# Kernel optimization log

Measured on AMD Instinct MI355X. Metric: run time of the kernel, lower is better.

## Reference

```python
import jax, jax.numpy as jnp
import numpy as np

B, N, DIM = 4, 1024, 768
H, HD = 12, DIM // 12
GP = 49
MLP = 3072


def _layernorm(x, w, b, eps=1e-5):
    mu = x.mean(axis=-1, keepdims=True)
    var = ((x - mu) ** 2).mean(axis=-1, keepdims=True)
    return (x - mu) * jax.lax.rsqrt(var + eps) * w + b


def setup_inputs() -> dict:
    key = jax.random.key(0)
    ks = jax.random.split(key, 12)
    s = 0.02
    return {
        "x": jax.random.normal(ks[0], (B, N, DIM), jnp.float32),
        "ln1_w": jnp.ones((DIM,), jnp.float32),
        "ln1_b": jnp.zeros((DIM,), jnp.float32),
        "qkv_w": jax.random.normal(ks[1], (DIM, 3 * DIM), jnp.float32) * s,
        "qkv_b": jnp.zeros((3 * DIM,), jnp.float32),
        "proj_w": jax.random.normal(ks[2], (DIM, DIM), jnp.float32) * s,
        "proj_b": jnp.zeros((DIM,), jnp.float32),
        "gp_w": jax.random.normal(ks[3], (GP, DIM), jnp.float32) * s,  # nn.Linear(dim, gp_num).weight, shape (gp_num, dim)
        "alpha": jax.random.normal(ks[4], (1, H, 1, 1), jnp.float32),
        "ln2_w": jnp.ones((DIM,), jnp.float32),
        "ln2_b": jnp.zeros((DIM,), jnp.float32),
        "ff1_w": jax.random.normal(ks[5], (DIM, MLP), jnp.float32) * s,
        "ff1_b": jnp.zeros((MLP,), jnp.float32),
        "ff2_w": jax.random.normal(ks[6], (MLP, DIM), jnp.float32) * s,
        "ff2_b": jnp.zeros((DIM,), jnp.float32),
    }


def reference(x, ln1_w, ln1_b, qkv_w, qkv_b, proj_w, proj_b, gp_w, alpha,
              ln2_w, ln2_b, ff1_w, ff1_b, ff2_w, ff2_b):
    b, n, _ = x.shape
    # --- attention branch ---
    xn = _layernorm(x, ln1_w, ln1_b)
    qkv = xn @ qkv_w + qkv_b                                 # [b,n,3*dim]
    q, k, v = jnp.split(qkv, 3, axis=-1)
    to_heads = lambda t: t.reshape(b, n, H, HD).transpose(0, 2, 1, 3)  # [b,h,n,hd]
    q, k, v = to_heads(q), to_heads(k), to_heads(v)
    scale = HD ** -0.5
    attn = jnp.einsum('bhnd,bhmd->bhnm', q, k) * scale       # raw scores
    # group weights: view (gp_num, dim) -> (h, gp_num, hd) (row-major, same as torch .view)
    gp = gp_w.reshape(H, GP, HD)
    gw = jnp.einsum('bhnd,hmd->bhnm', v, gp)                 # [b,h,n,gp]
    gw = jax.nn.gelu(gw, approximate=False)
    gw = jax.nn.softmax(gw, axis=-1)
    gw = jnp.einsum('bhnm,bhkm->bhnk', gw, gw)               # [b,h,n,n]
    attn = jax.nn.softmax(attn * gw, axis=-1)
    a = jax.nn.sigmoid(alpha)
    attn = (1.0 - a) * attn + a * gw
    attn = attn / (attn.sum(axis=2, keepdims=True) + 1e-8)   # note: dim=2 (column renorm), faithful to source
    out = jnp.einsum('bhnm,bhmd->bhnd', attn, v)
    out = out.transpose(0, 2, 1, 3).reshape(b, n, DIM)
    out = out @ proj_w + proj_b
    x = out + x
    # --- FFN branch ---
    xn = _layernorm(x, ln2_w, ln2_b)
    hdn = jax.nn.gelu(xn @ ff1_w + ff1_b, approximate=False)
    x = (hdn @ ff2_w + ff2_b) + x
    return x
```

## Files before the change

### kernel.cpp

```cpp
#include <hip/hip_runtime.h>
#include <hip/hip_bf16.h>
#include <math.h>

#define DEVI __device__ __forceinline__

typedef __bf16 bf16x8 __attribute__((ext_vector_type(8)));
typedef float f32x4 __attribute__((ext_vector_type(4)));
typedef unsigned int u32x4 __attribute__((ext_vector_type(4)));
typedef float f32x4v __attribute__((ext_vector_type(4)));
typedef unsigned short u16;

DEVI u16 f2bf(float f) {
    __hip_bfloat16 h = __float2bfloat16(f);
    return __builtin_bit_cast(u16, h);
}
DEVI float bf2f(u16 u) {
    unsigned int x = ((unsigned int)u) << 16;
    return __builtin_bit_cast(float, x);
}
DEVI float gelu_f(float x) {
    float y = 0.7978845608f * (x + 0.044715f * x * x * x);
    float e = __expf(2.f * y);
    float t = 1.f - 2.f / (e + 1.f);
    return 0.5f * x * (1.f + t);
}
DEVI float sigm(float x) { return 1.f / (1.f + __expf(-x)); }

DEVI bf16x8 ldfrag(const u16* p) {
    return __builtin_bit_cast(bf16x8, *reinterpret_cast<const u32x4*>(p));
}

DEVI void gload_lds16(const u16* g, u16* l) {
    __builtin_amdgcn_global_load_lds(
        (const __attribute__((address_space(1))) void*)g,
        (__attribute__((address_space(3))) void*)l, 16, 0, 0);
}

DEVI void stage8(const u16* gbase, long long stride, u16* lds, int lane) {
    int r = lane >> 3;
    int kg = (lane & 7) ^ r;
    gload_lds16(gbase + (long long)r * stride + kg * 8, lds);
}
DEVI bf16x8 fragsw(const u16* tile, int rr, int k) {
    return ldfrag(&tile[rr * 64 + ((k ^ (rr & 7)) << 3)]);
}

__global__ __launch_bounds__(256) void tcast_k(const float* __restrict__ in, u16* __restrict__ out,
                                               int R, int C) {
    __shared__ float tile[32][33];
    int c0 = blockIdx.x * 32, r0 = blockIdx.y * 32;
    for (int ry = threadIdx.y; ry < 32; ry += 8)
        tile[ry][threadIdx.x] = in[(long long)(r0 + ry) * C + c0 + threadIdx.x];
    __syncthreads();
    for (int cy = threadIdx.y; cy < 32; cy += 8)
        out[(long long)(c0 + cy) * R + r0 + threadIdx.x] = f2bf(tile[threadIdx.x][cy]);
}

__global__ __launch_bounds__(256) void ln_k(const float* __restrict__ parts, int nparts, long long pstride,
                                            const float* __restrict__ bias2, const float* __restrict__ in2,
                                            const float* __restrict__ w, const float* __restrict__ b,
                                            u16* __restrict__ outbf, float* __restrict__ x1out,
                                            float* __restrict__ zfill) {
    int row = blockIdx.x;
    if (zfill && row < 192) zfill[row * 256 + threadIdx.x] = 0.f;
    long long ro = (long long)row * 768;
    __shared__ float lds1[4], lds2[4];
    float v[3];
    float s = 0.f, sq = 0.f;
#pragma unroll
    for (int j = 0; j < 3; j++) {
        int c = threadIdx.x + j * 256;
        float x = 0.f;
        for (int p = 0; p < nparts; p++) x += parts[p * pstride + ro + c];
        if (bias2) x += bias2[c];
        if (in2) x += in2[ro + c];
        v[j] = x; s += x; sq += x * x;
    }
    if (x1out) {
#pragma unroll
        for (int j = 0; j < 3; j++) x1out[ro + threadIdx.x + j * 256] = v[j];
    }
    for (int off = 32; off; off >>= 1) { s += __shfl_down(s, off); sq += __shfl_down(sq, off); }
    int wid = threadIdx.x >> 6;
    if ((threadIdx.x & 63) == 0) { lds1[wid] = s; lds2[wid] = sq; }
    __syncthreads();
    s = lds1[0] + lds1[1] + lds1[2] + lds1[3];
    sq = lds2[0] + lds2[1] + lds2[2] + lds2[3];
    float mu = s * (1.f / 768.f);
    float var = sq * (1.f / 768.f) - mu * mu;
    float rs = rsqrtf(var + 1e-5f);
#pragma unroll
    for (int j = 0; j < 3; j++) {
        int c = threadIdx.x + j * 256;
        outbf[ro + c] = f2bf((v[j] - mu) * rs * w[c] + b[c]);
    }
}

struct GemmP {
    const u16* A; const u16* B;
    float* outF; u16* outB;
    const float* bias;
    u16* qh; u16* kh; u16* vh;
    int K, lda, ldb, ldc;
    long long pstride;
    int epi;
    int splits;
};

__global__ __launch_bounds__(128) void gemm_bt2(GemmP p) {
    __shared__ u16 As[64 * 64];
    __shared__ u16 Bs[128 * 64];
    const int tid = threadIdx.x, lane = tid & 63, wave = tid >> 6;
    const int l16 = lane & 15, qd = lane >> 4;
    const int bn0 = blockIdx.x * 128, bm0 = blockIdx.y * 64;
    const int wn0 = wave * 64;
    const int kc = p.K / p.splits;
    const int kbeg = blockIdx.z * kc, kend = kbeg + kc;
    f32x4 acc[4][4] = {};
    for (int k0 = kbeg; k0 < kend; k0 += 64) {
        __syncthreads();
#pragma unroll
        for (int t = 0; t < 4; t++) {
            int rowg = wave * 32 + t * 8;
            stage8(p.A + (long long)(bm0 + rowg) * p.lda + k0, p.lda, As + rowg * 64, lane);
        }
#pragma unroll
        for (int t = 0; t < 8; t++) {
            int rowg = wave * 64 + t * 8;
            stage8(p.B + (long long)(bn0 + rowg) * p.ldb + k0, p.ldb, Bs + rowg * 64, lane);
        }
        __syncthreads();
#pragma unroll
        for (int s = 0; s < 2; s++) {
            bf16x8 af[4], bv[4];
#pragma unroll
            for (int i = 0; i < 4; i++) af[i] = fragsw(As, i * 16 + l16, s * 4 + qd);
#pragma unroll
            for (int j = 0; j < 4; j++) bv[j] = fragsw(Bs, wn0 + j * 16 + l16, s * 4 + qd);
#pragma unroll
            for (int i = 0; i < 4; i++)
#pragma unroll
                for (int j = 0; j < 4; j++)
                    acc[i][j] = __builtin_amdgcn_mfma_f32_16x16x32_bf16(af[i], bv[j], acc[i][j], 0, 0, 0);
        }
    }
#pragma unroll
    for (int i = 0; i < 4; i++)
#pragma unroll
        for (int j = 0; j < 4; j++)
#pragma unroll
            for (int r = 0; r < 4; r++) {
                int row = bm0 + i * 16 + qd * 4 + r;
                int col = bn0 + wn0 + j * 16 + l16;
                float v = acc[i][j][r];
                if (p.epi == 0) {
                    p.outF[(long long)blockIdx.z * p.pstride + (long long)row * p.ldc + col] = v;
                } else if (p.epi == 2) {
                    p.outB[(long long)row * p.ldc + col] = f2bf(gelu_f(v + p.bias[col]));
                } else {
                    v += p.bias[col];
                    int sect = col / 768, cc = col % 768;
                    int h = cc >> 6, d = cc & 63;
                    int b = row >> 10, n = row & 1023;
                    long long o = ((long long)(b * 12 + h) * 1024 + n) * 64 + d;
                    if (sect == 0) p.qh[o] = f2bf(v * 0.125f);
                    else if (sect == 1) p.kh[o] = f2bf(v);
                    else p.vh[o] = f2bf(v);
                }
            }
}

__global__ __launch_bounds__(256) void gpcast_k(const float* __restrict__ gp_w, u16* __restrict__ gpB) {
    int h = blockIdx.x;
    for (int i = threadIdx.x; i < 4096; i += 256) {
        int m = i >> 6, d = i & 63;
        float v = (m < 49) ? gp_w[h * 3136 + m * 64 + d] : 0.f;
        gpB[h * 4096 + i] = f2bf(v);
    }
}

__global__ __launch_bounds__(256) void gw0m_k(const u16* __restrict__ vh, const u16* __restrict__ gpB,
                                              u16* __restrict__ gwn, float* __restrict__ Wt) {
    {
        long long zi = ((long long)blockIdx.y * 16 + blockIdx.x) * 256 + threadIdx.x;
        Wt[zi] = 0.f;
    }
    __shared__ u16 As[64 * 64];
    __shared__ u16 Bs[64 * 64];
    const int tid = threadIdx.x, lane = tid & 63, wave = tid >> 6;
    const int l16 = lane & 15, qd = lane >> 4;
    const int z = blockIdx.y, n0 = blockIdx.x * 64, h = z % 12;
    const u16* vz = vh + ((long long)z * 1024 + n0) * 64;
    const u16* gz = gpB + h * 4096;
#pragma unroll
    for (int t = 0; t < 2; t++) {
        int rowg = wave * 16 + t * 8;
        stage8(vz + (long long)rowg * 64, 64, As + rowg * 64, lane);
        stage8(gz + (long long)rowg * 64, 64, Bs + rowg * 64, lane);
    }
    __syncthreads();
    f32x4 acc[4] = {};
#pragma unroll
    for (int s = 0; s < 2; s++) {
        bf16x8 af = fragsw(As, wave * 16 + l16, s * 4 + qd);
#pragma unroll
        for (int j = 0; j < 4; j++) {
            bf16x8 bv = fragsw(Bs, j * 16 + l16, s * 4 + qd);
            acc[j] = __builtin_amdgcn_mfma_f32_16x16x32_bf16(af, bv, acc[j], 0, 0, 0);
        }
    }
    float ex[4][4];
#pragma unroll
    for (int r = 0; r < 4; r++) {
        float mx = -1e30f;
        float gv[4];
#pragma unroll
        for (int j = 0; j < 4; j++) {
            int col = j * 16 + l16;
            float g = gelu_f(acc[j][r]);
            gv[j] = g;
            if (col < 49) mx = fmaxf(mx, g);
            else gv[j] = -1e30f;
        }
        mx = fmaxf(mx, __shfl_xor(mx, 1)); mx = fmaxf(mx, __shfl_xor(mx, 2));
        mx = fmaxf(mx, __shfl_xor(mx, 4)); mx = fmaxf(mx, __shfl_xor(mx, 8));
        float s = 0.f;
#pragma unroll
        for (int j = 0; j < 4; j++) {
            int col = j * 16 + l16;
            float e = (col < 49) ? __expf(gv[j] - mx) : 0.f;
            ex[r][j] = e;
            s += e;
        }
        s += __shfl_xor(s, 1); s += __shfl_xor(s, 2);
        s += __shfl_xor(s, 4); s += __shfl_xor(s, 8);
        float inv = 1.f / s;
        int row = wave * 16 + qd * 4 + r;
        long long o = ((long long)z * 1024 + n0 + row) * 64;
#pragma unroll
        for (int j = 0; j < 4; j++)
            gwn[o + j * 16 + l16] = f2bf(ex[r][j] * inv);
    }
}

__global__ __launch_bounds__(256) void attn_tg4(const u16* __restrict__ qh, const u16* __restrict__ kh,
                                                const u16* __restrict__ gwn, u16* __restrict__ e,
                                                float* __restrict__ rowsumE) {
    __shared__ u16 As[128 * 64];
    __shared__ u16 Bs[128 * 64];
    const int tid = threadIdx.x, lane = tid & 63, wave = tid >> 6;
    const int l16 = lane & 15, qd = lane >> 4;
    const int bn0 = blockIdx.x * 128, bm0 = blockIdx.y * 128, z = blockIdx.z;
    const int wm0 = (wave >> 1) * 64, wn0 = (wave & 1) * 64;
    const u16* qz = qh + (long long)z * 65536;
    const u16* kz = kh + (long long)z * 65536;
    const u16* gz = gwn + (long long)z * 65536;
    f32x4 accS[4][4] = {};
    f32x4 accG[4][4] = {};
#pragma unroll
    for (int t = 0; t < 4; t++) {
        int rowg = wave * 32 + t * 8;
        stage8(qz + (long long)(bm0 + rowg) * 64, 64, As + rowg * 64, lane);
        stage8(kz + (long long)(bn0 + rowg) * 64, 64, Bs + rowg * 64, lane);
    }
    __syncthreads();
#pragma unroll
    for (int s = 0; s < 2; s++) {
        bf16x8 af[4], bv[4];
#pragma unroll
        for (int i = 0; i < 4; i++) af[i] = fragsw(As, wm0 + i * 16 + l16, s * 4 + qd);
#pragma unroll
        for (int j = 0; j < 4; j++) bv[j] = fragsw(Bs, wn0 + j * 16 + l16, s * 4 + qd);
#pragma unroll
        for (int i = 0; i < 4; i++)
#pragma unroll
            for (int j = 0; j < 4; j++)
                accS[i][j] = __builtin_amdgcn_mfma_f32_16x16x32_bf16(af[i], bv[j], accS[i][j], 0, 0, 0);
    }
    __syncthreads();
#pragma unroll
    for (int t = 0; t < 4; t++) {
        int rowg = wave * 32 + t * 8;
        stage8(gz + (long long)(bm0 + rowg) * 64, 64, As + rowg * 64, lane);
        stage8(gz + (long long)(bn0 + rowg) * 64, 64, Bs + rowg * 64, lane);
    }
    __syncthreads();
#pragma unroll
    for (int s = 0; s < 2; s++) {
        bf16x8 af[4], bv[4];
#pragma unroll
        for (int i = 0; i < 4; i++) af[i] = fragsw(As, wm0 + i * 16 + l16, s * 4 + qd);
#pragma unroll
        for (int j = 0; j < 4; j++) bv[j] = fragsw(Bs, wn0 + j * 16 + l16, s * 4 + qd);
#pragma unroll
        for (int i = 0; i < 4; i++)
#pragma unroll
            for (int j = 0; j < 4; j++)
                accG[i][j] = __builtin_amdgcn_mfma_f32_16x16x32_bf16(af[i], bv[j], accG[i][j], 0, 0, 0);
    }
    long long zoff = (long long)z * 1048576;
#pragma unroll
    for (int i = 0; i < 4; i++)
#pragma unroll
        for (int r = 0; r < 4; r++) {
            int row = bm0 + wm0 + i * 16 + qd * 4 + r;
            float rs = 0.f;
#pragma unroll
            for (int j = 0; j < 4; j++) {
                int col = bn0 + wn0 + j * 16 + l16;
                float ev = __expf(accS[i][j][r] * accG[i][j][r]);
                e[zoff + (long long)row * 1024 + col] = f2bf(ev);
                rs += ev;
            }
            rs += __shfl_xor(rs, 1); rs += __shfl_xor(rs, 2);
            rs += __shfl_xor(rs, 4); rs += __shfl_xor(rs, 8);
            if (l16 == 0) atomicAdd(&rowsumE[z * 1024 + row], rs);
        }
}

__global__ __launch_bounds__(256) void combine2_k(const u16* __restrict__ gwn, const float* __restrict__ alpha,
                                                  float* __restrict__ colsum) {
    int z = blockIdx.x, h = z % 12;
    int j = threadIdx.x & 63, part = threadIdx.x >> 6;
    __shared__ float lds[4][64];
    __shared__ float Sl[64];
    float s = 0.f;
    for (int i = 0; i < 256; i++)
        s += bf2f(gwn[((long long)z * 1024 + part * 256 + i) * 64 + j]);
    lds[part][j] = s;
    __syncthreads();
    if (threadIdx.x < 64)
        Sl[threadIdx.x] = lds[0][threadIdx.x] + lds[1][threadIdx.x] + lds[2][threadIdx.x] + lds[3][threadIdx.x];
    __syncthreads();
    float a = sigm(alpha[h]);
    for (int m = threadIdx.x; m < 1024; m += 256) {
        const u16* g = gwn + ((long long)z * 1024 + m) * 64;
        float dot = 0.f;
#pragma unroll 8
        for (int jj = 0; jj < 64; jj++) dot += bf2f(g[jj]) * Sl[jj];
        colsum[z * 1024 + m] = a * dot;
    }
}

__global__ __launch_bounds__(256) void colsumE_k(const u16* __restrict__ e, const float* __restrict__ rowsumE,
                                                 const float* __restrict__ alpha, float* __restrict__ colsum) {
    int z = blockIdx.x, h = z % 12;
    int n0 = blockIdx.y * 128;
    int grp = threadIdx.x & 127;
    int half = threadIdx.x >> 7;
    const u16* p = e + (long long)z * 1048576;
    const float* rs = rowsumE + z * 1024;
    float acc[8] = {};
    for (int n = n0 + half * 64; n < n0 + half * 64 + 64; n++) {
        unsigned int rw[4];
        *reinterpret_cast<u32x4*>(rw) = *reinterpret_cast<const u32x4*>(&p[(long long)n * 1024 + grp * 8]);
        float inv = 1.f / rs[n];
#pragma unroll
        for (int q = 0; q < 4; q++) {
            float lo = __builtin_bit_cast(float, rw[q] << 16);
            float hi = __builtin_bit_cast(float, rw[q] & 0xffff0000u);
            acc[2 * q] += lo * inv;
            acc[2 * q + 1] += hi * inv;
        }
    }
    __shared__ float part[2][128][8];
#pragma unroll
    for (int j = 0; j < 8; j++) part[half][grp][j] = acc[j];
    __syncthreads();
    if (half == 0) {
        float a = sigm(alpha[h]);
#pragma unroll
        for (int j = 0; j < 8; j++)
            atomicAdd(&colsum[z * 1024 + grp * 8 + j], (1.f - a) * (part[0][grp][j] + part[1][grp][j]));
    }
}

__global__ __launch_bounds__(256) void vpt_k(const u16* __restrict__ vh, const float* __restrict__ colsum,
                                             u16* __restrict__ vpt) {
    int z = blockIdx.y, m0 = blockIdx.x * 64;
    __shared__ float ts[64 * 65];
    int mi = threadIdx.x >> 6, d = threadIdx.x & 63;
    for (int rr = 0; rr < 16; rr++) {
        int row = rr * 4 + mi;
        ts[row * 65 + d] = bf2f(vh[((long long)z * 1024 + m0 + row) * 64 + d]);
    }
    __syncthreads();
    int mj = threadIdx.x & 63, d0 = threadIdx.x >> 6;
    for (int rr = 0; rr < 16; rr++) {
        int dd = rr * 4 + d0;
        float cs = colsum[z * 1024 + m0 + mj] + 1e-8f;
        vpt[((long long)z * 64 + dd) * 1024 + m0 + mj] = f2bf(ts[mj * 65 + dd] / cs);
    }
}

__global__ __launch_bounds__(256) void wgemm_k(const u16* __restrict__ gwn, const u16* __restrict__ vpt,
                                               float* __restrict__ Wt) {
    int z = blockIdx.y, n0 = blockIdx.x * 128;
    __shared__ u16 gs[128 * 64];
    __shared__ u16 vs2[64 * 128];
    for (int i = threadIdx.x; i < 128 * 64; i += 256) {
        int nn = i >> 6, j = i & 63;
        gs[i] = gwn[((long long)z * 1024 + n0 + nn) * 64 + j];
        int d = i >> 7, n2 = i & 127;
        vs2[i] = vpt[((long long)z * 64 + d) * 1024 + n0 + n2];
    }
    __syncthreads();
    int j = threadIdx.x & 63, dg = threadIdx.x >> 6;
    float acc[16] = {};
    for (int nn = 0; nn < 128; nn++) {
        float g = bf2f(gs[nn * 64 + j]);
#pragma unroll
        for (int i = 0; i < 16; i++) acc[i] += g * bf2f(vs2[(dg * 16 + i) * 128 + nn]);
    }
#pragma unroll
    for (int i = 0; i < 16; i++)
        atomicAdd(&Wt[((long long)z * 64 + dg * 16 + i) * 64 + j], acc[i]);
}

__global__ __launch_bounds__(256) void attn_out4(const u16* __restrict__ e, const u16* __restrict__ vpt,
                                                 const u16* __restrict__ gwn, const float* __restrict__ Wt,
                                                 const float* __restrict__ rowsumE,
                                                 const float* __restrict__ alpha, u16* __restrict__ out) {
    __shared__ u16 As[64 * 64];
    __shared__ u16 Bs[64 * 64];
    const int tid = threadIdx.x, lane = tid & 63, wave = tid >> 6;
    const int l16 = lane & 15, qd = lane >> 4;
    const int bm0 = blockIdx.x * 64, z = blockIdx.y;
    const int h = z % 12, b = z / 12;
    const u16* Pz = e + (long long)z * 1048576;
    const u16* vz = vpt + (long long)z * 65536;
    const int wr = wave * 16;
    f32x4 accP[4] = {};
    f32x4 accG[4] = {};
    for (int k0 = 0; k0 < 1024; k0 += 64) {
        __syncthreads();
#pragma unroll
        for (int t = 0; t < 2; t++) {
            int rowg = wave * 16 + t * 8;
            stage8(Pz + (long long)(bm0 + rowg) * 1024 + k0, 1024, As + rowg * 64, lane);
            stage8(vz + (long long)rowg * 1024 + k0, 1024, Bs + rowg * 64, lane);
        }
        __syncthreads();
#pragma unroll
        for (int s = 0; s < 2; s++) {
            bf16x8 af = fragsw(As, wr + l16, s * 4 + qd);
#pragma unroll
            for (int j = 0; j < 4; j++) {
                bf16x8 bv = fragsw(Bs, j * 16 + l16, s * 4 + qd);
                accP[j] = __builtin_amdgcn_mfma_f32_16x16x32_bf16(af, bv, accP[j], 0, 0, 0);
            }
        }
    }
    const u16* gz = gwn + (long long)z * 65536;
    const float* wz = Wt + (long long)z * 4096;
    __syncthreads();
#pragma unroll
    for (int t = 0; t < 2; t++) {
        int rowg = wave * 16 + t * 8;
        stage8(gz + (long long)(bm0 + rowg) * 64, 64, As + rowg * 64, lane);
    }
    {
        int row = tid >> 2, c0 = (tid & 3) * 16;
        const float* wrow = wz + row * 64;
#pragma unroll
        for (int j0 = 0; j0 < 16; j0++) {
            int j = c0 + j0;
            int pos = (((j >> 3) ^ (row & 7)) << 3) | (j & 7);
            Bs[row * 64 + pos] = f2bf(wrow[j]);
        }
    }
    __syncthreads();
#pragma unroll
    for (int s = 0; s < 2; s++) {
        bf16x8 af = fragsw(As, wr + l16, s * 4 + qd);
#pragma unroll
        for (int j = 0; j < 4; j++) {
            bf16x8 bv = fragsw(Bs, j * 16 + l16, s * 4 + qd);
            accG[j] = __builtin_amdgcn_mfma_f32_16x16x32_bf16(af, bv, accG[j], 0, 0, 0);
        }
    }
    float a = sigm(alpha[h]);
#pragma unroll
    for (int r = 0; r < 4; r++) {
        int n = bm0 + wr + qd * 4 + r;
        float sc = (1.f - a) / rowsumE[z * 1024 + n];
#pragma unroll
        for (int j = 0; j < 4; j++) {
            int d = j * 16 + l16;
            float v = sc * accP[j][r] + a * accG[j][r];
            out[((long long)(b * 1024 + n)) * 768 + h * 64 + d] = f2bf(v);
        }
    }
}

__global__ __launch_bounds__(256) void fuse2_k(const float* __restrict__ parts, long long pstride4,
                                               const float* __restrict__ bias, const float* __restrict__ x1,
                                               float* __restrict__ outp) {
    long long i4 = (long long)blockIdx.x * 256 + threadIdx.x;
    int c4 = (int)(i4 % 192);
    const f32x4v* p0 = (const f32x4v*)parts;
    f32x4v v = p0[i4] + p0[pstride4 + i4];
    f32x4v bb = ((const f32x4v*)bias)[c4];
    f32x4v xx = ((const f32x4v*)x1)[i4];
    ((f32x4v*)outp)[i4] = v + bb + xx;
}

extern "C" void kernel_launch(void* const* d_in, const int* in_sizes, int n_in,
                              void* d_out, int out_size, void* d_ws, size_t ws_size,
                              hipStream_t stream) {
    const float* x      = (const float*)d_in[0];
    const float* ln1_w  = (const float*)d_in[1];
    const float* ln1_b  = (const float*)d_in[2];
    const float* qkv_w  = (const float*)d_in[3];
    const float* qkv_b  = (const float*)d_in[4];
    const float* proj_w = (const float*)d_in[5];
    const float* proj_b = (const float*)d_in[6];
    const float* gp_w   = (const float*)d_in[7];
    const float* alpha  = (const float*)d_in[8];
    const float* ln2_w  = (const float*)d_in[9];
    const float* ln2_b  = (const float*)d_in[10];
    const float* ff1_w  = (const float*)d_in[11];
    const float* ff1_b  = (const float*)d_in[12];
    const float* ff2_w  = (const float*)d_in[13];
    const float* ff2_b  = (const float*)d_in[14];

    char* w = (char*)d_ws;
    size_t off = 0;
    auto alloc = [&](size_t bytes) { size_t r = off; off += (bytes + 255) & ~(size_t)255; return r; };

    u16*   xn_bf   = (u16*)(w + alloc(4096LL * 768 * 2));
    u16*   wqkv_t  = (u16*)(w + alloc(2304LL * 768 * 2));
    u16*   wproj_t = (u16*)(w + alloc(768LL * 768 * 2));
    u16*   wff1_t  = (u16*)(w + alloc(3072LL * 768 * 2));
    u16*   wff2_t  = (u16*)(w + alloc(768LL * 3072 * 2));
    u16*   gpB     = (u16*)(w + alloc(12LL * 64 * 64 * 2));
    u16*   qh      = (u16*)(w + alloc(48LL * 1024 * 64 * 2));
    u16*   kh      = (u16*)(w + alloc(48LL * 1024 * 64 * 2));
    u16*   vh      = (u16*)(w + alloc(48LL * 1024 * 64 * 2));
    u16*   gwn     = (u16*)(w + alloc(48LL * 1024 * 64 * 2));
    u16*   ebuf    = (u16*)(w + alloc(48LL * 1024 * 1024 * 2));
    float* rowsumE = (float*)(w + alloc(48LL * 1024 * 4));
    float* Wt      = (float*)(w + alloc(48LL * 64 * 64 * 4));
    float* colsum  = (float*)(w + alloc(48LL * 1024 * 4));
    u16*   vpt     = (u16*)(w + alloc(48LL * 64 * 1024 * 2));
    float* x1      = (float*)(w + alloc(4096LL * 768 * 4));
    u16*   attn_o  = (u16*)(w + alloc(4096LL * 768 * 2));
    u16*   xn2     = (u16*)(w + alloc(4096LL * 768 * 2));
    float* projP = (float*)ebuf;
    u16*   hmid  = (u16*)((char*)ebuf + 2 * 4096LL * 768 * 4);
    float* ff2P  = (float*)((char*)ebuf + 2 * 4096LL * 768 * 4 + 4096LL * 3072 * 2);

    dim3 blk(256);
    dim3 blk2(128);
    const long long PS = 4096LL * 768;

    tcast_k<<<dim3(72, 24), dim3(32, 8), 0, stream>>>(qkv_w, wqkv_t, 768, 2304);
    tcast_k<<<dim3(24, 24), dim3(32, 8), 0, stream>>>(proj_w, wproj_t, 768, 768);
    tcast_k<<<dim3(96, 24), dim3(32, 8), 0, stream>>>(ff1_w, wff1_t, 768, 3072);
    tcast_k<<<dim3(24, 96), dim3(32, 8), 0, stream>>>(ff2_w, wff2_t, 3072, 768);
    gpcast_k<<<dim3(12), blk, 0, stream>>>(gp_w, gpB);

    ln_k<<<dim3(4096), blk, 0, stream>>>(x, 1, 0, nullptr, nullptr, ln1_w, ln1_b, xn_bf, nullptr, rowsumE);

    {
        GemmP p = {xn_bf, wqkv_t, nullptr, nullptr, qkv_b, qh, kh, vh, 768, 768, 768, 0, 0, 4, 1};
        gemm_bt2<<<dim3(18, 64, 1), blk2, 0, stream>>>(p);
    }

    gw0m_k<<<dim3(16, 48), blk, 0, stream>>>(vh, gpB, gwn, Wt);

    attn_tg4<<<dim3(8, 8, 48), blk, 0, stream>>>(qh, kh, gwn, ebuf, rowsumE);

    combine2_k<<<dim3(48), blk, 0, stream>>>(gwn, alpha, colsum);
    colsumE_k<<<dim3(48, 8), blk, 0, stream>>>(ebuf, rowsumE, alpha, colsum);

    vpt_k<<<dim3(16, 48), blk, 0, stream>>>(vh, colsum, vpt);

    wgemm_k<<<dim3(8, 48), blk, 0, stream>>>(gwn, vpt, Wt);

    attn_out4<<<dim3(16, 48), blk, 0, stream>>>(ebuf, vpt, gwn, Wt, rowsumE, alpha, attn_o);

    {
        GemmP p = {attn_o, wproj_t, projP, nullptr, nullptr, nullptr, nullptr, nullptr,
                   768, 768, 768, 768, PS, 0, 2};
        gemm_bt2<<<dim3(6, 64, 2), blk2, 0, stream>>>(p);
    }

    ln_k<<<dim3(4096), blk, 0, stream>>>(projP, 2, PS, proj_b, x, ln2_w, ln2_b, xn2, x1, nullptr);

    {
        GemmP p = {xn2, wff1_t, nullptr, hmid, ff1_b, nullptr, nullptr, nullptr,
                   768, 768, 768, 3072, 0, 2, 1};
        gemm_bt2<<<dim3(24, 64, 1), blk2, 0, stream>>>(p);
    }

    {
        GemmP p = {hmid, wff2_t, ff2P, nullptr, nullptr, nullptr, nullptr, nullptr,
                   3072, 3072, 3072, 768, PS, 0, 2};
        gemm_bt2<<<dim3(6, 64, 2), blk2, 0, stream>>>(p);
    }

    fuse2_k<<<dim3(3072), blk, 0, stream>>>(ff2P, PS / 4, ff2_b, x1, (float*)d_out);
}
```

Before: 487.3 us.

## Store exp scores in fp8, enlarge GEMM tiles, merge weight-cast kernels

The unnormalized exp(score*gw) matrix is now stored as fp8 instead of bf16, halving the dominant 48x1024x1024 buffer traffic. Its consumers decode the fp8 in registers, and attn_out4 converts it to bf16 before staging into LDS. The GEMM kernel moves from a 64x128 tile with 128 threads to a 128x128 tile with 256 threads, and the five weight transpose/cast launches are merged into one. The fp8 encoding loses precision on attention weights, which risks accuracy, and attn_out4 now does a synchronous register-path load instead of the async global-to-LDS path.

New measurement: 466.0 us. 1.05x faster.

```diff
diff --git a/kernel.cpp b/kernel.cpp
--- a/kernel.cpp
+++ b/kernel.cpp
@@ -6,9 +6,11 @@
 
 typedef __bf16 bf16x8 __attribute__((ext_vector_type(8)));
 typedef float f32x4 __attribute__((ext_vector_type(4)));
+typedef float f32x2 __attribute__((ext_vector_type(2)));
 typedef unsigned int u32x4 __attribute__((ext_vector_type(4)));
 typedef float f32x4v __attribute__((ext_vector_type(4)));
 typedef unsigned short u16;
+typedef unsigned char u8;
 
 DEVI u16 f2bf(float f) {
     __hip_bfloat16 h = __float2bfloat16(f);
@@ -45,10 +47,35 @@
     return ldfrag(&tile[rr * 64 + ((k ^ (rr & 7)) << 3)]);
 }
 
-__global__ __launch_bounds__(256) void tcast_k(const float* __restrict__ in, u16* __restrict__ out,
-                                               int R, int C) {
+DEVI unsigned int packbf(float a, float b) {
+    return __builtin_amdgcn_perm(__builtin_bit_cast(unsigned int, b),
+                                 __builtin_bit_cast(unsigned int, a), 0x07060302u);
+}
+
+__global__ __launch_bounds__(256) void tcast_all(const float* __restrict__ qkv_w, const float* __restrict__ proj_w,
+                                                 const float* __restrict__ ff1_w, const float* __restrict__ ff2_w,
+                                                 const float* __restrict__ gp_w,
+                                                 u16* __restrict__ wqkv, u16* __restrict__ wproj,
+                                                 u16* __restrict__ wff1, u16* __restrict__ wff2,
+                                                 u16* __restrict__ gpB) {
+    int id = blockIdx.x;
+    if (id >= 6912) {
+        int h = id - 6912;
+        int tid = threadIdx.y * 32 + threadIdx.x;
+        for (int i = tid; i < 4096; i += 256) {
+            int m = i >> 6, d = i & 63;
+            float v = (m < 49) ? gp_w[h * 3136 + m * 64 + d] : 0.f;
+            gpB[h * 4096 + i] = f2bf(v);
+        }
+        return;
+    }
+    const float* in; u16* out; int R, C, tx;
+    if (id < 1728)      { in = qkv_w;  out = wqkv;  R = 768;  C = 2304; tx = 72; }
+    else if (id < 2304) { in = proj_w; out = wproj; R = 768;  C = 768;  tx = 24; id -= 1728; }
+    else if (id < 4608) { in = ff1_w;  out = wff1;  R = 768;  C = 3072; tx = 96; id -= 2304; }
+    else                { in = ff2_w;  out = wff2;  R = 3072; C = 768;  tx = 24; id -= 4608; }
+    int c0 = (id % tx) * 32, r0 = (id / tx) * 32;
     __shared__ float tile[32][33];
-    int c0 = blockIdx.x * 32, r0 = blockIdx.y * 32;
     for (int ry = threadIdx.y; ry < 32; ry += 8)
         tile[ry][threadIdx.x] = in[(long long)(r0 + ry) * C + c0 + threadIdx.x];
     __syncthreads();
@@ -107,13 +134,13 @@
     int splits;
 };
 
-__global__ __launch_bounds__(128) void gemm_bt2(GemmP p) {
-    __shared__ u16 As[64 * 64];
+__global__ __launch_bounds__(256) void gemm_bt4(GemmP p) {
+    __shared__ u16 As[128 * 64];
     __shared__ u16 Bs[128 * 64];
     const int tid = threadIdx.x, lane = tid & 63, wave = tid >> 6;
     const int l16 = lane & 15, qd = lane >> 4;
-    const int bn0 = blockIdx.x * 128, bm0 = blockIdx.y * 64;
-    const int wn0 = wave * 64;
+    const int bn0 = blockIdx.x * 128, bm0 = blockIdx.y * 128;
+    const int wm0 = (wave >> 1) * 64, wn0 = (wave & 1) * 64;
     const int kc = p.K / p.splits;
     const int kbeg = blockIdx.z * kc, kend = kbeg + kc;
     f32x4 acc[4][4] = {};
@@ -123,10 +150,6 @@
         for (int t = 0; t < 4; t++) {
             int rowg = wave * 32 + t * 8;
             stage8(p.A + (long long)(bm0 + rowg) * p.lda + k0, p.lda, As + rowg * 64, lane);
-        }
-#pragma unroll
-        for (int t = 0; t < 8; t++) {
-            int rowg = wave * 64 + t * 8;
             stage8(p.B + (long long)(bn0 + rowg) * p.ldb + k0, p.ldb, Bs + rowg * 64, lane);
         }
         __syncthreads();
@@ -134,7 +157,7 @@
         for (int s = 0; s < 2; s++) {
             bf16x8 af[4], bv[4];
 #pragma unroll
-            for (int i = 0; i < 4; i++) af[i] = fragsw(As, i * 16 + l16, s * 4 + qd);
+            for (int i = 0; i < 4; i++) af[i] = fragsw(As, wm0 + i * 16 + l16, s * 4 + qd);
 #pragma unroll
             for (int j = 0; j < 4; j++) bv[j] = fragsw(Bs, wn0 + j * 16 + l16, s * 4 + qd);
 #pragma unroll
@@ -150,7 +173,7 @@
         for (int j = 0; j < 4; j++)
 #pragma unroll
             for (int r = 0; r < 4; r++) {
-                int row = bm0 + i * 16 + qd * 4 + r;
+                int row = bm0 + wm0 + i * 16 + qd * 4 + r;
                 int col = bn0 + wn0 + j * 16 + l16;
                 float v = acc[i][j][r];
                 if (p.epi == 0) {
@@ -170,15 +193,6 @@
             }
 }
 
-__global__ __launch_bounds__(256) void gpcast_k(const float* __restrict__ gp_w, u16* __restrict__ gpB) {
-    int h = blockIdx.x;
-    for (int i = threadIdx.x; i < 4096; i += 256) {
-        int m = i >> 6, d = i & 63;
-        float v = (m < 49) ? gp_w[h * 3136 + m * 64 + d] : 0.f;
-        gpB[h * 4096 + i] = f2bf(v);
-    }
-}
-
 __global__ __launch_bounds__(256) void gw0m_k(const u16* __restrict__ vh, const u16* __restrict__ gpB,
                                               u16* __restrict__ gwn, float* __restrict__ Wt) {
     {
@@ -244,7 +258,7 @@
 }
 
 __global__ __launch_bounds__(256) void attn_tg4(const u16* __restrict__ qh, const u16* __restrict__ kh,
-                                                const u16* __restrict__ gwn, u16* __restrict__ e,
+                                                const u16* __restrict__ gwn, u8* __restrict__ e8,
                                                 float* __restrict__ rowsumE) {
     __shared__ u16 As[128 * 64];
     __shared__ u16 Bs[128 * 64];
@@ -309,7 +323,8 @@
             for (int j = 0; j < 4; j++) {
                 int col = bn0 + wn0 + j * 16 + l16;
                 float ev = __expf(accS[i][j][r] * accG[i][j][r]);
-                e[zoff + (long long)row * 1024 + col] = f2bf(ev);
+                unsigned int pk = (unsigned int)__builtin_amdgcn_cvt_pk_fp8_f32(ev, ev, 0, false);
+                e8[zoff + (long long)row * 1024 + col] = (u8)(pk & 0xff);
                 rs += ev;
             }
             rs += __shfl_xor(rs, 1); rs += __shfl_xor(rs, 2);
@@ -342,26 +357,27 @@
     }
 }
 
-__global__ __launch_bounds__(256) void colsumE_k(const u16* __restrict__ e, const float* __restrict__ rowsumE,
+__global__ __launch_bounds__(256) void colsumE_k(const u8* __restrict__ e8, const float* __restrict__ rowsumE,
                                                  const float* __restrict__ alpha, float* __restrict__ colsum) {
     int z = blockIdx.x, h = z % 12;
     int n0 = blockIdx.y * 128;
     int grp = threadIdx.x & 127;
     int half = threadIdx.x >> 7;
-    const u16* p = e + (long long)z * 1048576;
+    const u8* p = e8 + (long long)z * 1048576;
     const float* rs = rowsumE + z * 1024;
     float acc[8] = {};
     for (int n = n0 + half * 64; n < n0 + half * 64 + 64; n++) {
-        unsigned int rw[4];
-        *reinterpret_cast<u32x4*>(rw) = *reinterpret_cast<const u32x4*>(&p[(long long)n * 1024 + grp * 8]);
+        unsigned long long w8 = *reinterpret_cast<const unsigned long long*>(&p[(long long)n * 1024 + grp * 8]);
+        unsigned int w0 = (unsigned int)w8, w1 = (unsigned int)(w8 >> 32);
         float inv = 1.f / rs[n];
-#pragma unroll
-        for (int q = 0; q < 4; q++) {
-            float lo = __builtin_bit_cast(float, rw[q] << 16);
-            float hi = __builtin_bit_cast(float, rw[q] & 0xffff0000u);
-            acc[2 * q] += lo * inv;
-            acc[2 * q + 1] += hi * inv;
-        }
+        f32x2 a0 = __builtin_amdgcn_cvt_pk_f32_fp8((int)w0, false);
+        f32x2 a1 = __builtin_amdgcn_cvt_pk_f32_fp8((int)w0, true);
+        f32x2 a2 = __builtin_amdgcn_cvt_pk_f32_fp8((int)w1, false);
+        f32x2 a3 = __builtin_amdgcn_cvt_pk_f32_fp8((int)w1, true);
+        acc[0] += a0.x * inv; acc[1] += a0.y * inv;
+        acc[2] += a1.x * inv; acc[3] += a1.y * inv;
+        acc[4] += a2.x * inv; acc[5] += a2.y * inv;
+        acc[6] += a3.x * inv; acc[7] += a3.y * inv;
     }
     __shared__ float part[2][128][8];
 #pragma unroll
@@ -417,7 +433,7 @@
         atomicAdd(&Wt[((long long)z * 64 + dg * 16 + i) * 64 + j], acc[i]);
 }
 
-__global__ __launch_bounds__(256) void attn_out4(const u16* __restrict__ e, const u16* __restrict__ vpt,
+__global__ __launch_bounds__(256) void attn_out4(const u8* __restrict__ e8, const u16* __restrict__ vpt,
                                                  const u16* __restrict__ gwn, const float* __restrict__ Wt,
                                                  const float* __restrict__ rowsumE,
                                                  const float* __restrict__ alpha, u16* __restrict__ out) {
@@ -427,17 +443,33 @@
     const int l16 = lane & 15, qd = lane >> 4;
     const int bm0 = blockIdx.x * 64, z = blockIdx.y;
     const int h = z % 12, b = z / 12;
-    const u16* Pz = e + (long long)z * 1048576;
+    const u8* Pz = e8 + (long long)z * 1048576;
     const u16* vz = vpt + (long long)z * 65536;
     const int wr = wave * 16;
     f32x4 accP[4] = {};
     f32x4 accG[4] = {};
+    const int arow = wr + (lane >> 2);
+    const int cp = (lane & 3) * 2;
     for (int k0 = 0; k0 < 1024; k0 += 64) {
         __syncthreads();
+        {
+            u32x4 wv = *reinterpret_cast<const u32x4*>(Pz + (long long)(bm0 + arow) * 1024 + k0 + cp * 8);
+            unsigned int ob[8];
+#pragma unroll
+            for (int k = 0; k < 4; k++) {
+                f32x2 lo = __builtin_amdgcn_cvt_pk_f32_fp8((int)wv[k], false);
+                f32x2 hi = __builtin_amdgcn_cvt_pk_f32_fp8((int)wv[k], true);
+                ob[2 * k]     = packbf(lo.x, lo.y);
+                ob[2 * k + 1] = packbf(hi.x, hi.y);
+            }
+            int p0 = (cp ^ (arow & 7)) << 3;
+            int p1 = ((cp + 1) ^ (arow & 7)) << 3;
+            *reinterpret_cast<u32x4*>(&As[arow * 64 + p0]) = *reinterpret_cast<u32x4*>(&ob[0]);
+            *reinterpret_cast<u32x4*>(&As[arow * 64 + p1]) = *reinterpret_cast<u32x4*>(&ob[4]);
+        }
 #pragma unroll
         for (int t = 0; t < 2; t++) {
             int rowg = wave * 16 + t * 8;
-            stage8(Pz + (long long)(bm0 + rowg) * 1024 + k0, 1024, As + rowg * 64, lane);
             stage8(vz + (long long)rowg * 1024 + k0, 1024, Bs + rowg * 64, lane);
         }
         __syncthreads();
@@ -538,7 +570,8 @@
     u16*   kh      = (u16*)(w + alloc(48LL * 1024 * 64 * 2));
     u16*   vh      = (u16*)(w + alloc(48LL * 1024 * 64 * 2));
     u16*   gwn     = (u16*)(w + alloc(48LL * 1024 * 64 * 2));
-    u16*   ebuf    = (u16*)(w + alloc(48LL * 1024 * 1024 * 2));
+    char*  ebase   = w + alloc(2 * 4096LL * 768 * 4 + 4096LL * 3072 * 2 + 2 * 4096LL * 768 * 4);
+    u8*    e8      = (u8*)ebase;
     float* rowsumE = (float*)(w + alloc(48LL * 1024 * 4));
     float* Wt      = (float*)(w + alloc(48LL * 64 * 64 * 4));
     float* colsum  = (float*)(w + alloc(48LL * 1024 * 4));
@@ -546,44 +579,40 @@
     float* x1      = (float*)(w + alloc(4096LL * 768 * 4));
     u16*   attn_o  = (u16*)(w + alloc(4096LL * 768 * 2));
     u16*   xn2     = (u16*)(w + alloc(4096LL * 768 * 2));
-    float* projP = (float*)ebuf;
-    u16*   hmid  = (u16*)((char*)ebuf + 2 * 4096LL * 768 * 4);
-    float* ff2P  = (float*)((char*)ebuf + 2 * 4096LL * 768 * 4 + 4096LL * 3072 * 2);
+    float* projP = (float*)ebase;
+    u16*   hmid  = (u16*)(ebase + 2 * 4096LL * 768 * 4);
+    float* ff2P  = (float*)(ebase + 2 * 4096LL * 768 * 4 + 4096LL * 3072 * 2);
 
     dim3 blk(256);
-    dim3 blk2(128);
     const long long PS = 4096LL * 768;
 
-    tcast_k<<<dim3(72, 24), dim3(32, 8), 0, stream>>>(qkv_w, wqkv_t, 768, 2304);
-    tcast_k<<<dim3(24, 24), dim3(32, 8), 0, stream>>>(proj_w, wproj_t, 768, 768);
-    tcast_k<<<dim3(96, 24), dim3(32, 8), 0, stream>>>(ff1_w, wff1_t, 768, 3072);
-    tcast_k<<<dim3(24, 96), dim3(32, 8), 0, stream>>>(ff2_w, wff2_t, 3072, 768);
-    gpcast_k<<<dim3(12), blk, 0, stream>>>(gp_w, gpB);
+    tcast_all<<<dim3(6924), dim3(32, 8), 0, stream>>>(qkv_w, proj_w, ff1_w, ff2_w, gp_w,
+                                                      wqkv_t, wproj_t, wff1_t, wff2_t, gpB);
 
     ln_k<<<dim3(4096), blk, 0, stream>>>(x, 1, 0, nullptr, nullptr, ln1_w, ln1_b, xn_bf, nullptr, rowsumE);
 
     {
         GemmP p = {xn_bf, wqkv_t, nullptr, nullptr, qkv_b, qh, kh, vh, 768, 768, 768, 0, 0, 4, 1};
-        gemm_bt2<<<dim3(18, 64, 1), blk2, 0, stream>>>(p);
+        gemm_bt4<<<dim3(18, 32, 1), blk, 0, stream>>>(p);
     }
 
     gw0m_k<<<dim3(16, 48), blk, 0, stream>>>(vh, gpB, gwn, Wt);
 
-    attn_tg4<<<dim3(8, 8, 48), blk, 0, stream>>>(qh, kh, gwn, ebuf, rowsumE);
+    attn_tg4<<<dim3(8, 8, 48), blk, 0, stream>>>(qh, kh, gwn, e8, rowsumE);
 
     combine2_k<<<dim3(48), blk, 0, stream>>>(gwn, alpha, colsum);
-    colsumE_k<<<dim3(48, 8), blk, 0, stream>>>(ebuf, rowsumE, alpha, colsum);
+    colsumE_k<<<dim3(48, 8), blk, 0, stream>>>(e8, rowsumE, alpha, colsum);
 
     vpt_k<<<dim3(16, 48), blk, 0, stream>>>(vh, colsum, vpt);
 
     wgemm_k<<<dim3(8, 48), blk, 0, stream>>>(gwn, vpt, Wt);
 
-    attn_out4<<<dim3(16, 48), blk, 0, stream>>>(ebuf, vpt, gwn, Wt, rowsumE, alpha, attn_o);
+    attn_out4<<<dim3(16, 48), blk, 0, stream>>>(e8, vpt, gwn, Wt, rowsumE, alpha, attn_o);
 
     {
         GemmP p = {attn_o, wproj_t, projP, nullptr, nullptr, nullptr, nullptr, nullptr,
                    768, 768, 768, 768, PS, 0, 2};
-        gemm_bt2<<<dim3(6, 64, 2), blk2, 0, stream>>>(p);
+        gemm_bt4<<<dim3(6, 32, 2), blk, 0, stream>>>(p);
     }
 
     ln_k<<<dim3(4096), blk, 0, stream>>>(projP, 2, PS, proj_b, x, ln2_w, ln2_b, xn2, x1, nullptr);
@@ -591,13 +620,13 @@
     {
         GemmP p = {xn2, wff1_t, nullptr, hmid, ff1_b, nullptr, nullptr, nullptr,
                    768, 768, 768, 3072, 0, 2, 1};
-        gemm_bt2<<<dim3(24, 64, 1), blk2, 0, stream>>>(p);
+        gemm_bt4<<<dim3(24, 32, 1), blk, 0, stream>>>(p);
     }
 
     {
         GemmP p = {hmid, wff2_t, ff2P, nullptr, nullptr, nullptr, nullptr, nullptr,
                    3072, 3072, 3072, 768, PS, 0, 2};
-        gemm_bt2<<<dim3(6, 64, 2), blk2, 0, stream>>>(p);
+        gemm_bt4<<<dim3(6, 32, 2), blk, 0, stream>>>(p);
     }
 
     fuse2_k<<<dim3(3072), blk, 0, stream>>>(ff2P, PS / 4, ff2_b, x1, (float*)d_out);
```
